# Optimization experiments

Measured on AMD Instinct MI355X. Metric: run time of the kernel, lower is better.

Reference implementation:

```python
import jax, jax.numpy as jnp
import numpy as np
import math

B, N, OBS, ACT = 128, 64, 128, 16
D = OBS + ACT          # obs_act_input_dim = 144
DK = 128               # obs_act_output_dim (d_k)
ENC = 128              # encoder_output_dim
FIN = 1                # final_output_dim


def setup_inputs() -> dict:
    key = jax.random.key(0)
    ks = jax.random.split(key, 8)
    s = 0.05
    return {
        "observations": jax.random.normal(ks[0], (B, N, OBS), jnp.float32),
        "policies": jax.random.uniform(ks[1], (B, N, ACT), jnp.float32),
        "actions": jax.random.uniform(ks[2], (B, N, ACT), jnp.float32),
        # torch nn.Linear weights are [out, in]
        "Wk": jax.random.normal(ks[3], (DK, D), jnp.float32) * s,
        "Wq": jax.random.normal(ks[4], (DK, D), jnp.float32) * s,
        "Wv": jax.random.normal(ks[5], (DK, D), jnp.float32) * s,
        "Wenc": jax.random.normal(ks[6], (ENC, OBS), jnp.float32) * s,
        "Wfin": jax.random.normal(ks[7], (FIN, ENC + DK), jnp.float32) * s,
    }


def reference(observations, policies, actions, Wk, Wq, Wv, Wenc, Wfin):
    b, n = observations.shape[0], observations.shape[1]
    d_k = Wk.shape[0]
    oa = jnp.concatenate([observations, actions], axis=-1)      # [B,N,D]
    op = jnp.concatenate([observations, policies], axis=-1)     # [B,N,D]
    k = oa @ Wk.T                                               # [B,N,dk]
    q = oa @ Wq.T                                               # [B,N,dk]
    # torch: bmm(q, k^T).transpose(1,2) -> scores[b,i,j] = q[b,j] . k[b,i]
    scores = jnp.einsum('bjd,bid->bij', q, k)
    w = jax.nn.sigmoid(scores / math.sqrt(d_k))                 # [B,N,N]
    Va = oa @ Wv.T                                              # [B,N,dk] value of obs||action
    Vp = op @ Wv.T                                              # [B,N,dk] value of obs||policy
    # original 5D masked combine reduces to: agg[b,i,m] = (sum_j w[b,i,j]*Va[b,j]
    #   + w[b,i,m]*(Vp[b,m]-Va[b,m])) / N  (policy substituted only where j==m)
    S = jnp.einsum('bij,bjd->bid', w, Va)                       # [B,N,dk]
    agg = (S[:, :, None, :] + w[..., None] * (Vp - Va)[:, None, :, :]) / n  # [B,N,N,dk]
    enc = observations @ Wenc.T                                 # [B,N,ENC]
    enc_rep = jnp.broadcast_to(enc[:, :, None, :], (b, n, n, enc.shape[-1]))
    node = jnp.concatenate([enc_rep, agg], axis=-1)             # [B,N,N,ENC+dk]
    value = node @ Wfin.T                                       # [B,N,N,1]
    weights5 = jnp.broadcast_to(w[:, :, None, :, None], (b, n, n, n, 1))
    return value, weights5
```

## Files before the change

### kernel.cpp

```cpp
#include <hip/hip_runtime.h>
#include <stdint.h>


#define BB 128
#define NN 64
#define OBSD 128
#define ACTD 16
#define DD 144
#define DKD 128

typedef float f32x4 __attribute__((ext_vector_type(4)));

#define WS_QT  1048576
#define WS_VAS 2097152
#define WS_VE  (WS_VAS + 8192)
#define WS_DV  (WS_VAS + 16384)

__global__ __launch_bounds__(512, 2) void critic_kq(
    const float* __restrict__ obs, const float* __restrict__ pol, const float* __restrict__ act,
    const float* __restrict__ Wk, const float* __restrict__ Wq, const float* __restrict__ Wv,
    const float* __restrict__ Wenc, const float* __restrict__ Wfin,
    float* __restrict__ ws)
{
  __shared__ __align__(16) float s_oa[NN][148];
  __shared__ __align__(16) float s_W[DKD][148];
  __shared__ float s_dpa[NN][ACTD];
  __shared__ float s_u[DD];
  __shared__ float s_g[OBSD];

  const int tid = threadIdx.x;
  const int b = blockIdx.x >> 1;
  const int half = blockIdx.x & 1;

  {
    const float4* obs4 = (const float4*)(obs + (size_t)b * NN * OBSD);
    for (int idx = tid; idx < NN * OBSD / 4; idx += 512) {
      int i = idx >> 5, d0 = (idx & 31) * 4;
      *(float4*)&s_oa[i][d0] = obs4[idx];
    }
    const float4* act4 = (const float4*)(act + (size_t)b * NN * ACTD);
    const float4* pol4 = (const float4*)(pol + (size_t)b * NN * ACTD);
    for (int idx = tid; idx < NN * ACTD / 4; idx += 512) {
      float4 a = act4[idx];
      int i = idx >> 2, t0 = (idx & 3) * 4;
      *(float4*)&s_oa[i][OBSD + t0] = a;
      if (half == 0) {
        float4 p = pol4[idx];
        s_dpa[i][t0 + 0] = p.x - a.x; s_dpa[i][t0 + 1] = p.y - a.y;
        s_dpa[i][t0 + 2] = p.z - a.z; s_dpa[i][t0 + 3] = p.w - a.w;
      }
    }
  }
  {
    const float4* W4 = (const float4*)(half ? Wq : Wk);
    for (int idx = tid; idx < DKD * DD / 4; idx += 512) {
      int row = idx / 36, col = (idx - row * 36) * 4;
      *(float4*)&s_W[row][col] = W4[idx];
    }
  }
  if (half == 0) {
    if (tid < DD) {
      float a0=0.f,a1=0.f,a2=0.f,a3=0.f,a4=0.f,a5=0.f,a6=0.f,a7=0.f;
      for (int c = 0; c < DKD; c += 8) {
        a0 += Wv[(size_t)(c+0)*DD + tid] * Wfin[OBSD + c + 0];
        a1 += Wv[(size_t)(c+1)*DD + tid] * Wfin[OBSD + c + 1];
        a2 += Wv[(size_t)(c+2)*DD + tid] * Wfin[OBSD + c + 2];
        a3 += Wv[(size_t)(c+3)*DD + tid] * Wfin[OBSD + c + 3];
        a4 += Wv[(size_t)(c+4)*DD + tid] * Wfin[OBSD + c + 4];
        a5 += Wv[(size_t)(c+5)*DD + tid] * Wfin[OBSD + c + 5];
        a6 += Wv[(size_t)(c+6)*DD + tid] * Wfin[OBSD + c + 6];
        a7 += Wv[(size_t)(c+7)*DD + tid] * Wfin[OBSD + c + 7];
      }
      s_u[tid] = ((a0+a1)+(a2+a3)) + ((a4+a5)+(a6+a7));
    } else if (tid < DD + OBSD) {
      const int d = tid - DD;
      float a0=0.f,a1=0.f,a2=0.f,a3=0.f,a4=0.f,a5=0.f,a6=0.f,a7=0.f;
      for (int c = 0; c < 128; c += 8) {
        a0 += Wenc[(size_t)(c+0)*OBSD + d] * Wfin[c + 0];
        a1 += Wenc[(size_t)(c+1)*OBSD + d] * Wfin[c + 1];
        a2 += Wenc[(size_t)(c+2)*OBSD + d] * Wfin[c + 2];
        a3 += Wenc[(size_t)(c+3)*OBSD + d] * Wfin[c + 3];
        a4 += Wenc[(size_t)(c+4)*OBSD + d] * Wfin[c + 4];
        a5 += Wenc[(size_t)(c+5)*OBSD + d] * Wfin[c + 5];
        a6 += Wenc[(size_t)(c+6)*OBSD + d] * Wfin[c + 6];
        a7 += Wenc[(size_t)(c+7)*OBSD + d] * Wfin[c + 7];
      }
      s_g[d] = ((a0+a1)+(a2+a3)) + ((a4+a5)+(a6+a7));
    }
  }
  __syncthreads();

  const int cl = tid & 63;
  const int ig = tid >> 6;
  float acc0[8], acc1[8];
  #pragma unroll
  for (int r = 0; r < 8; ++r) { acc0[r] = 0.f; acc1[r] = 0.f; }
  #pragma unroll 4
  for (int d0 = 0; d0 < DD; d0 += 4) {
    float4 w0 = *(const float4*)&s_W[cl][d0];
    float4 w1 = *(const float4*)&s_W[cl + 64][d0];
    #pragma unroll
    for (int r = 0; r < 8; ++r) {
      float4 o = *(const float4*)&s_oa[ig * 8 + r][d0];
      acc0[r] += o.x * w0.x + o.y * w0.y + o.z * w0.z + o.w * w0.w;
      acc1[r] += o.x * w1.x + o.y * w1.y + o.z * w1.z + o.w * w1.w;
    }
  }

  if (half == 0) {
    float* kb = ws + (size_t)b * 8192;
    #pragma unroll
    for (int r = 0; r < 8; ++r) {
      kb[(ig * 8 + r) * 128 + cl]      = acc0[r];
      kb[(ig * 8 + r) * 128 + cl + 64] = acc1[r];
    }
    if (tid < 64) {
      float a = 0.f;
      for (int d = 0; d < DD; ++d) a += s_oa[tid][d] * s_u[d];
      ws[WS_VAS + b * 64 + tid] = a;
    } else if (tid < 128) {
      const int i = tid - 64;
      float a = 0.f;
      for (int d = 0; d < OBSD; ++d) a += s_oa[i][d] * s_g[d];
      ws[WS_VE + b * 64 + i] = a;
    } else if (tid < 192) {
      const int i = tid - 128;
      float a = 0.f;
      #pragma unroll
      for (int t = 0; t < ACTD; ++t) a += s_dpa[i][t] * s_u[OBSD + t];
      ws[WS_DV + b * 64 + i] = a;
    }
  } else {
    float* qb = ws + WS_QT + (size_t)b * 8192;
    #pragma unroll
    for (int r = 0; r < 8; ++r) {
      qb[cl * 64 + ig * 8 + r]        = acc0[r];
      qb[(cl + 64) * 64 + ig * 8 + r] = acc1[r];
    }
  }
}

__global__ __launch_bounds__(256, 2) void critic_sw(
    const float* __restrict__ ws, float* __restrict__ out)
{
  __shared__ __align__(16) float s_qT[DKD][64];
  __shared__ __align__(16) float s_k[16][132];
  __shared__ __align__(16) float s_w[16][68];
  __shared__ float s_vas[64], s_dv[64], s_ve[16], s_sv[16];

  const int t = threadIdx.x;
  const int b = blockIdx.x >> 2;
  const int i0 = (blockIdx.x & 3) * 16;

  {
    const float4* qt4 = (const float4*)(ws + WS_QT + (size_t)b * 8192);
    for (int idx = t; idx < 2048; idx += 256) {
      int c = idx >> 4, i4 = (idx & 15) * 4;
      *(float4*)&s_qT[c][i4] = qt4[idx];
    }
    const float4* k4 = (const float4*)(ws + (size_t)b * 8192 + (size_t)i0 * 128);
    for (int idx = t; idx < 512; idx += 256) {
      int r = idx >> 5, c4 = (idx & 31) * 4;
      *(float4*)&s_k[r][c4] = k4[idx];
    }
    if (t < 64)            s_vas[t] = ws[WS_VAS + b * 64 + t];
    else if (t < 128)      s_dv[t - 64] = ws[WS_DV + b * 64 + (t - 64)];
    else if (t < 144)      s_ve[t - 128] = ws[WS_VE + b * 64 + i0 + (t - 128)];
  }
  __syncthreads();

  {
    const int wv = t >> 6, j = t & 63;
    float sc0 = 0.f, sc1 = 0.f, sc2 = 0.f, sc3 = 0.f;
    #pragma unroll 4
    for (int d0 = 0; d0 < DKD; d0 += 4) {
      float q0 = s_qT[d0 + 0][j], q1 = s_qT[d0 + 1][j];
      float q2 = s_qT[d0 + 2][j], q3 = s_qT[d0 + 3][j];
      float4 k0 = *(const float4*)&s_k[wv * 4 + 0][d0];
      float4 k1 = *(const float4*)&s_k[wv * 4 + 1][d0];
      float4 k2 = *(const float4*)&s_k[wv * 4 + 2][d0];
      float4 k3 = *(const float4*)&s_k[wv * 4 + 3][d0];
      sc0 += k0.x * q0 + k0.y * q1 + k0.z * q2 + k0.w * q3;
      sc1 += k1.x * q0 + k1.y * q1 + k1.z * q2 + k1.w * q3;
      sc2 += k2.x * q0 + k2.y * q1 + k2.z * q2 + k2.w * q3;
      sc3 += k3.x * q0 + k3.y * q1 + k3.z * q2 + k3.w * q3;
    }
    const float kk = 0.08838834764831845f;
    s_w[wv * 4 + 0][j] = 1.0f / (1.0f + __expf(-sc0 * kk));
    s_w[wv * 4 + 1][j] = 1.0f / (1.0f + __expf(-sc1 * kk));
    s_w[wv * 4 + 2][j] = 1.0f / (1.0f + __expf(-sc2 * kk));
    s_w[wv * 4 + 3][j] = 1.0f / (1.0f + __expf(-sc3 * kk));
  }
  __syncthreads();

  if (t < 16) {
    float a = 0.f;
    for (int j = 0; j < 64; ++j) a += s_w[t][j] * s_vas[j];
    s_sv[t] = a;
  }
  __syncthreads();

  {
    const int r = t >> 4, m4 = (t & 15) * 4;
    float4 v;
    v.x = s_ve[r] + (s_sv[r] + s_w[r][m4 + 0] * s_dv[m4 + 0]) * (1.0f / 64.0f);
    v.y = s_ve[r] + (s_sv[r] + s_w[r][m4 + 1] * s_dv[m4 + 1]) * (1.0f / 64.0f);
    v.z = s_ve[r] + (s_sv[r] + s_w[r][m4 + 2] * s_dv[m4 + 2]) * (1.0f / 64.0f);
    v.w = s_ve[r] + (s_sv[r] + s_w[r][m4 + 3] * s_dv[m4 + 3]) * (1.0f / 64.0f);
    *(float4*)(out + ((size_t)(b * 64 + i0 + r) * 64 + m4)) = v;
  }

  float* w5 = out + (size_t)BB * NN * NN;
  #pragma unroll 4
  for (int r = 0; r < 16; ++r) {
    const f32x4 wv4 = *(const f32x4*)&s_w[r][(t & 15) * 4];
    f32x4* p4 = (f32x4*)(w5 + ((size_t)(b * 64 + i0 + r) << 12));
    __builtin_nontemporal_store(wv4, &p4[t]);
    __builtin_nontemporal_store(wv4, &p4[t + 256]);
    __builtin_nontemporal_store(wv4, &p4[t + 512]);
    __builtin_nontemporal_store(wv4, &p4[t + 768]);
  }
}

extern "C" void kernel_launch(void* const* d_in, const int* in_sizes, int n_in,
                              void* d_out, int out_size, void* d_ws, size_t ws_size,
                              hipStream_t stream) {
  (void)in_sizes; (void)n_in; (void)out_size; (void)ws_size;
  const float* obs  = (const float*)d_in[0];
  const float* pol  = (const float*)d_in[1];
  const float* act  = (const float*)d_in[2];
  const float* Wk   = (const float*)d_in[3];
  const float* Wq   = (const float*)d_in[4];
  const float* Wv   = (const float*)d_in[5];
  const float* Wenc = (const float*)d_in[6];
  const float* Wfin = (const float*)d_in[7];
  float* out = (float*)d_out;
  float* ws  = (float*)d_ws;
  hipLaunchKernelGGL(critic_kq, dim3(BB * 2), dim3(512), 0, stream,
                     obs, pol, act, Wk, Wq, Wv, Wenc, Wfin, ws);
  hipLaunchKernelGGL(critic_sw, dim3(BB * 4), dim3(256), 0, stream, ws, out);
}
```

Measured before the change: 193.2 us.

## Compute K/Q projections with bf16 MFMA instead of fp32 FMA loops

Result: faster. 179.4 us (-7.1%).

```diff
diff --git a/kernel.cpp b/kernel.cpp
--- a/kernel.cpp
+++ b/kernel.cpp
@@ -8,13 +8,25 @@
 #define ACTD 16
 #define DD 144
 #define DKD 128
+#define RS 168
 
 typedef float f32x4 __attribute__((ext_vector_type(4)));
+typedef short bf16x8 __attribute__((ext_vector_type(8)));
 
 #define WS_QT  1048576
 #define WS_VAS 2097152
 #define WS_VE  (WS_VAS + 8192)
 #define WS_DV  (WS_VAS + 16384)
+
+__device__ __forceinline__ unsigned int pack_bf2(float x, float y) {
+  unsigned a = __float_as_uint(x), b = __float_as_uint(y);
+  a = (a + 0x7fffu + ((a >> 16) & 1u)) >> 16;
+  b = (b + 0x7fffu + ((b >> 16) & 1u)) >> 16;
+  return a | (b << 16);
+}
+__device__ __forceinline__ float bf2f(unsigned short s) {
+  return __uint_as_float(((unsigned)s) << 16);
+}
 
 __global__ __launch_bounds__(512, 2) void critic_kq(
     const float* __restrict__ obs, const float* __restrict__ pol, const float* __restrict__ act,
@@ -22,8 +34,8 @@
     const float* __restrict__ Wenc, const float* __restrict__ Wfin,
     float* __restrict__ ws)
 {
-  __shared__ __align__(16) float s_oa[NN][148];
-  __shared__ __align__(16) float s_W[DKD][148];
+  __shared__ __align__(16) unsigned short s_A[NN * RS];
+  __shared__ __align__(16) unsigned short s_B[DKD * RS];
   __shared__ float s_dpa[NN][ACTD];
   __shared__ float s_u[DD];
   __shared__ float s_g[OBSD];
@@ -34,28 +46,44 @@
 
   {
     const float4* obs4 = (const float4*)(obs + (size_t)b * NN * OBSD);
-    for (int idx = tid; idx < NN * OBSD / 4; idx += 512) {
-      int i = idx >> 5, d0 = (idx & 31) * 4;
-      *(float4*)&s_oa[i][d0] = obs4[idx];
+    for (int idx = tid; idx < 2048; idx += 512) {
+      float4 v = obs4[idx];
+      int row = idx >> 5, c4 = (idx & 31) * 4;
+      *(uint2*)&s_A[row * RS + c4] = make_uint2(pack_bf2(v.x, v.y), pack_bf2(v.z, v.w));
     }
     const float4* act4 = (const float4*)(act + (size_t)b * NN * ACTD);
     const float4* pol4 = (const float4*)(pol + (size_t)b * NN * ACTD);
-    for (int idx = tid; idx < NN * ACTD / 4; idx += 512) {
+    for (int idx = tid; idx < 256; idx += 512) {
       float4 a = act4[idx];
-      int i = idx >> 2, t0 = (idx & 3) * 4;
-      *(float4*)&s_oa[i][OBSD + t0] = a;
+      int row = idx >> 2, c4 = OBSD + (idx & 3) * 4;
+      *(uint2*)&s_A[row * RS + c4] = make_uint2(pack_bf2(a.x, a.y), pack_bf2(a.z, a.w));
       if (half == 0) {
         float4 p = pol4[idx];
-        s_dpa[i][t0 + 0] = p.x - a.x; s_dpa[i][t0 + 1] = p.y - a.y;
-        s_dpa[i][t0 + 2] = p.z - a.z; s_dpa[i][t0 + 3] = p.w - a.w;
-      }
+        int t0 = (idx & 3) * 4;
+        s_dpa[row][t0 + 0] = p.x - a.x; s_dpa[row][t0 + 1] = p.y - a.y;
+        s_dpa[row][t0 + 2] = p.z - a.z; s_dpa[row][t0 + 3] = p.w - a.w;
+      }
+    }
+    for (int idx = tid; idx < 256; idx += 512) {
+      int row = idx >> 2, c4 = DD + (idx & 3) * 4;
+      *(uint2*)&s_A[row * RS + c4] = make_uint2(0u, 0u);
     }
   }
   {
     const float4* W4 = (const float4*)(half ? Wq : Wk);
-    for (int idx = tid; idx < DKD * DD / 4; idx += 512) {
-      int row = idx / 36, col = (idx - row * 36) * 4;
-      *(float4*)&s_W[row][col] = W4[idx];
+    for (int idx = tid; idx < 4096; idx += 512) {
+      int row = idx >> 5, g = idx & 31;
+      float4 v = W4[row * 36 + g];
+      *(uint2*)&s_B[row * RS + g * 4] = make_uint2(pack_bf2(v.x, v.y), pack_bf2(v.z, v.w));
+    }
+    for (int idx = tid; idx < 512; idx += 512) {
+      int row = idx >> 2, g = idx & 3;
+      float4 v = W4[row * 36 + 32 + g];
+      *(uint2*)&s_B[row * RS + OBSD + g * 4] = make_uint2(pack_bf2(v.x, v.y), pack_bf2(v.z, v.w));
+    }
+    for (int idx = tid; idx < 512; idx += 512) {
+      int row = idx >> 2, c4 = DD + (idx & 3) * 4;
+      *(uint2*)&s_B[row * RS + c4] = make_uint2(0u, 0u);
     }
   }
   if (half == 0) {
@@ -90,38 +118,48 @@
   }
   __syncthreads();
 
-  const int cl = tid & 63;
-  const int ig = tid >> 6;
-  float acc0[8], acc1[8];
-  #pragma unroll
-  for (int r = 0; r < 8; ++r) { acc0[r] = 0.f; acc1[r] = 0.f; }
-  #pragma unroll 4
-  for (int d0 = 0; d0 < DD; d0 += 4) {
-    float4 w0 = *(const float4*)&s_W[cl][d0];
-    float4 w1 = *(const float4*)&s_W[cl + 64][d0];
+  {
+    const int wv = tid >> 6, lane = tid & 63;
+    const int i0 = (wv & 3) * 16;
+    const int n0 = (wv >> 2) * 4;
+    const int m = lane & 15, q = lane >> 4;
+    f32x4 acc[4];
     #pragma unroll
-    for (int r = 0; r < 8; ++r) {
-      float4 o = *(const float4*)&s_oa[ig * 8 + r][d0];
-      acc0[r] += o.x * w0.x + o.y * w0.y + o.z * w0.z + o.w * w0.w;
-      acc1[r] += o.x * w1.x + o.y * w1.y + o.z * w1.z + o.w * w1.w;
+    for (int t = 0; t < 4; ++t) acc[t] = (f32x4){0.f, 0.f, 0.f, 0.f};
+    #pragma unroll
+    for (int ks = 0; ks < 5; ++ks) {
+      const int koff = ks * 32 + q * 8;
+      bf16x8 a = *(const bf16x8*)&s_A[(i0 + m) * RS + koff];
+      #pragma unroll
+      for (int t = 0; t < 4; ++t) {
+        bf16x8 bb = *(const bf16x8*)&s_B[((n0 + t) * 16 + m) * RS + koff];
+        acc[t] = __builtin_amdgcn_mfma_f32_16x16x32_bf16(a, bb, acc[t], 0, 0, 0);
+      }
+    }
+    if (half == 0) {
+      float* kb = ws + (size_t)b * 8192;
+      #pragma unroll
+      for (int t = 0; t < 4; ++t)
+        #pragma unroll
+        for (int r = 0; r < 4; ++r)
+          kb[(i0 + q * 4 + r) * 128 + (n0 + t) * 16 + m] = acc[t][r];
+    } else {
+      float* qb = ws + WS_QT + (size_t)b * 8192;
+      #pragma unroll
+      for (int t = 0; t < 4; ++t)
+        *(f32x4*)&qb[((n0 + t) * 16 + m) * 64 + i0 + q * 4] = acc[t];
     }
   }
 
   if (half == 0) {
-    float* kb = ws + (size_t)b * 8192;
-    #pragma unroll
-    for (int r = 0; r < 8; ++r) {
-      kb[(ig * 8 + r) * 128 + cl]      = acc0[r];
-      kb[(ig * 8 + r) * 128 + cl + 64] = acc1[r];
-    }
     if (tid < 64) {
       float a = 0.f;
-      for (int d = 0; d < DD; ++d) a += s_oa[tid][d] * s_u[d];
+      for (int d = 0; d < DD; ++d) a += bf2f(s_A[tid * RS + d]) * s_u[d];
       ws[WS_VAS + b * 64 + tid] = a;
     } else if (tid < 128) {
       const int i = tid - 64;
       float a = 0.f;
-      for (int d = 0; d < OBSD; ++d) a += s_oa[i][d] * s_g[d];
+      for (int d = 0; d < OBSD; ++d) a += bf2f(s_A[i * RS + d]) * s_g[d];
       ws[WS_VE + b * 64 + i] = a;
     } else if (tid < 192) {
       const int i = tid - 128;
@@ -129,13 +167,6 @@
       #pragma unroll
       for (int t = 0; t < ACTD; ++t) a += s_dpa[i][t] * s_u[OBSD + t];
       ws[WS_DV + b * 64 + i] = a;
-    }
-  } else {
-    float* qb = ws + WS_QT + (size_t)b * 8192;
-    #pragma unroll
-    for (int r = 0; r < 8; ++r) {
-      qb[cl * 64 + ig * 8 + r]        = acc0[r];
-      qb[(cl + 64) * 64 + ig * 8 + r] = acc1[r];
     }
   }
 }
```
